# Optimization experiments

Hardware: AMD Instinct MI355X
Metric: run time of the kernel (lower is better)

The kernel has to match this reference:

```python
import jax, jax.numpy as jnp
import numpy as np

NEG_SLOPE = 0.2  # PyG GATConv default negative_slope
BN_EPS = 1e-5


def _segment_softmax(logits, seg, num_segments):
    # numerically stable softmax over edges grouped by destination node
    m = jax.ops.segment_max(logits, seg, num_segments=num_segments)
    e = jnp.exp(logits - m[seg])
    s = jax.ops.segment_sum(e, seg, num_segments=num_segments)
    return e / s[seg]


def _gat_conv(x, src, dst, W, a_src, a_dst, bias, heads, d_head, concat):
    N = x.shape[0]
    h = (x @ W).reshape(N, heads, d_head)                      # [N, H, D]
    alpha_src = jnp.einsum('nhd,hd->nh', h, a_src)             # [N, H]
    alpha_dst = jnp.einsum('nhd,hd->nh', h, a_dst)             # [N, H]
    logits = jax.nn.leaky_relu(alpha_src[src] + alpha_dst[dst], NEG_SLOPE)  # [E, H]
    alpha = _segment_softmax(logits, dst, N)                   # [E, H]
    msg = h[src] * alpha[:, :, None]                           # [E, H, D]
    out = jax.ops.segment_sum(msg, dst, num_segments=N)        # [N, H, D]
    out = out.reshape(N, heads * d_head) if concat else out.mean(axis=1)
    return out + bias


def setup_inputs() -> dict:
    key = jax.random.key(0)
    ks = jax.random.split(key, 12)
    N, E = 50000, 800000
    in_dim, hidden, out_dim, heads = 256, 128, 2, 4
    d1 = hidden // heads  # 32
    s = 0.05
    return {
        'x': jax.random.normal(ks[0], (N, in_dim), dtype=jnp.float32),
        'edge_index': jax.random.randint(ks[1], (2, E), 0, N, dtype=jnp.int64),
        'W1': jax.random.normal(ks[2], (in_dim, heads * d1), dtype=jnp.float32) * s,
        'att_src1': jax.random.normal(ks[3], (heads, d1), dtype=jnp.float32) * s,
        'att_dst1': jax.random.normal(ks[4], (heads, d1), dtype=jnp.float32) * s,
        'b1': jnp.zeros((heads * d1,), dtype=jnp.float32),
        'bn_gamma': jnp.ones((hidden,), dtype=jnp.float32),
        'bn_beta': jnp.zeros((hidden,), dtype=jnp.float32),
        'bn_mean': jnp.zeros((hidden,), dtype=jnp.float32),
        'bn_var': jnp.ones((hidden,), dtype=jnp.float32),
        'W2': jax.random.normal(ks[5], (hidden, out_dim), dtype=jnp.float32) * s,
        'att_src2': jax.random.normal(ks[6], (1, out_dim), dtype=jnp.float32) * s,
        'att_dst2': jax.random.normal(ks[7], (1, out_dim), dtype=jnp.float32) * s,
        'b2': jnp.zeros((out_dim,), dtype=jnp.float32),
    }


def reference(x, edge_index, W1, att_src1, att_dst1, b1,
              bn_gamma, bn_beta, bn_mean, bn_var,
              W2, att_src2, att_dst2, b2):
    N = x.shape[0]
    # PyG GATConv adds self-loops by default
    loop = jnp.arange(N, dtype=edge_index.dtype)
    src = jnp.concatenate([edge_index[0], loop])
    dst = jnp.concatenate([edge_index[1], loop])

    heads, d1 = att_src1.shape
    h = _gat_conv(x, src, dst, W1, att_src1, att_dst1, b1, heads, d1, concat=True)
    # BatchNorm1d in eval mode (running stats), then ReLU (dropout is a no-op in eval)
    h = (h - bn_mean) * jax.lax.rsqrt(bn_var + BN_EPS) * bn_gamma + bn_beta
    h = jax.nn.relu(h)
    out = _gat_conv(h, src, dst, W2, att_src2, att_dst2, b2, 1, att_src2.shape[1], concat=False)
    return out
```

## Files before the change

### kernel.cpp

```cpp
#include <hip/hip_runtime.h>
#include <hip/hip_bf16.h>

#define LRELU(x) ((x) > 0.f ? (x) : 0.2f * (x))
#define CAP 96
#define BINBITS 7
#define BINCAP 2600

typedef short bf16x8 __attribute__((ext_vector_type(8)));
typedef float f32x4 __attribute__((ext_vector_type(4)));

__device__ __forceinline__ float b2f(unsigned short u) {
  union { unsigned int i; float f; } v;
  v.i = ((unsigned int)u) << 16;
  return v.f;
}
__device__ __forceinline__ unsigned short f2b(float f) {
  unsigned int u = __float_as_uint(f);
  unsigned int r = (u + 0x7fffu + ((u >> 16) & 1u)) >> 16;
  return (unsigned short)r;
}

__device__ __forceinline__ void acc2(float w, unsigned int p, float& a0,
                                     float& a1) {
  union { unsigned int u; float f; } lo, hi;
  lo.u = p << 16;
  hi.u = p & 0xffff0000u;
  a0 = fmaf(w, lo.f, a0);
  a1 = fmaf(w, hi.f, a1);
}

__global__ __launch_bounds__(256) void prep_w1t_kernel(
    const float* __restrict__ W, unsigned short* __restrict__ w1t) {
  int idx = blockIdx.x * 256 + threadIdx.x;
  int n = idx >> 8, k = idx & 255;
  w1t[idx] = f2b(W[k * 128 + n]);
}

__global__ __launch_bounds__(256) void gemm1_mfma_kernel(
    const float* __restrict__ x, const unsigned short* __restrict__ w1t,
    const float* __restrict__ atts, const float* __restrict__ attd,
    unsigned short* __restrict__ h1bf, float* __restrict__ asrc,
    float* __restrict__ adst, int N) {
  __shared__ unsigned short bsh[128 * 264];

  const int tid = threadIdx.x;
#pragma unroll
  for (int i = 0; i < 16; i++) {
    int idx = (i * 256 + tid) * 8;
    int row = idx >> 8;
    int k = idx & 255;
    *(uint4*)(bsh + row * 264 + k) = *(const uint4*)(w1t + row * 256 + k);
  }
  __syncthreads();

  const int m0 = blockIdx.x * 64 + (tid >> 6) * 16;
  if (m0 >= N) return;
  const int lane = tid & 63;
  const int row = lane & 15;
  const int quad = lane >> 4;

  f32x4 acc[8];
#pragma unroll
  for (int t = 0; t < 8; t++) acc[t] = (f32x4){0.f, 0.f, 0.f, 0.f};

  const float* ap = x + (size_t)(m0 + row) * 256 + quad * 8;
#pragma unroll
  for (int k0 = 0; k0 < 256; k0 += 32) {
    float4 av0 = *(const float4*)(ap + k0);
    float4 av1 = *(const float4*)(ap + k0 + 4);
    float af[8] = {av0.x, av0.y, av0.z, av0.w, av1.x, av1.y, av1.z, av1.w};
    bf16x8 ahi, alo;
#pragma unroll
    for (int j = 0; j < 8; j++) {
      unsigned short h = f2b(af[j]);
      ahi[j] = (short)h;
      alo[j] = (short)f2b(af[j] - b2f(h));
    }
#pragma unroll
    for (int t = 0; t < 8; t++) {
      bf16x8 b = *(const bf16x8*)(bsh + (t * 16 + row) * 264 + k0 + quad * 8);
      acc[t] = __builtin_amdgcn_mfma_f32_16x16x32_bf16(ahi, b, acc[t], 0, 0, 0);
      acc[t] = __builtin_amdgcn_mfma_f32_16x16x32_bf16(alo, b, acc[t], 0, 0, 0);
    }
  }
  unsigned short* op = h1bf + (size_t)(m0 + quad * 4) * 128 + row;
#pragma unroll
  for (int t = 0; t < 8; t++)
#pragma unroll
    for (int r = 0; r < 4; r++)
      op[(size_t)r * 128 + t * 16] = f2b(acc[t][r]);

  float asv[8], adv[8];
#pragma unroll
  for (int t = 0; t < 8; t++) {
    asv[t] = atts[t * 16 + row];
    adv[t] = attd[t * 16 + row];
  }
  float ps[4][4], pd[4][4];
#pragma unroll
  for (int h = 0; h < 4; h++)
#pragma unroll
    for (int r = 0; r < 4; r++) {
      ps[h][r] = acc[2 * h][r] * asv[2 * h] + acc[2 * h + 1][r] * asv[2 * h + 1];
      pd[h][r] = acc[2 * h][r] * adv[2 * h] + acc[2 * h + 1][r] * adv[2 * h + 1];
    }
#pragma unroll
  for (int o = 1; o < 16; o <<= 1) {
#pragma unroll
    for (int h = 0; h < 4; h++)
#pragma unroll
      for (int r = 0; r < 4; r++) {
        ps[h][r] += __shfl_xor(ps[h][r], o);
        pd[h][r] += __shfl_xor(pd[h][r], o);
      }
  }
  if (row == 0) {
#pragma unroll
    for (int r = 0; r < 4; r++) {
      int m = m0 + quad * 4 + r;
#pragma unroll
      for (int h = 0; h < 4; h++) {
        asrc[m * 4 + h] = ps[h][r];
        adst[m * 4 + h] = pd[h][r];
      }
    }
  }
}

__global__ __launch_bounds__(256) void bin_edges_kernel(
    const int* __restrict__ ei, int E, int* __restrict__ gcnt,
    unsigned int* __restrict__ binned, int nbins) {
  __shared__ int hist[512];
  __shared__ int base[512];
  const int tid = threadIdx.x;
  for (int i = tid; i < 512; i += 256) hist[i] = 0;
  __syncthreads();
  const int chunk = (E + gridDim.x - 1) / gridDim.x;
  const int e0 = blockIdx.x * chunk;
  const int e1 = min(e0 + chunk, E);
  for (int e = e0 + tid; e < e1; e += 256)
    atomicAdd(&hist[ei[(size_t)E + e] >> BINBITS], 1);
  __syncthreads();
  for (int i = tid; i < nbins; i += 256)
    if (hist[i] > 0) base[i] = atomicAdd(&gcnt[i], hist[i]);
  __syncthreads();
  for (int i = tid; i < 512; i += 256) hist[i] = 0;
  __syncthreads();
  for (int e = e0 + tid; e < e1; e += 256) {
    int s = ei[e];
    int t = ei[(size_t)E + e];
    int b = t >> BINBITS;
    int pos = base[b] + atomicAdd(&hist[b], 1);
    if (pos < BINCAP)
      binned[(size_t)b * BINCAP + pos] = ((unsigned int)t << 16) | (unsigned int)s;
  }
}

__global__ __launch_bounds__(256) void bin_to_buckets_kernel(
    const int* __restrict__ gcnt, const unsigned int* __restrict__ binned,
    int* __restrict__ cnt, unsigned short* __restrict__ buckets, int N) {
  __shared__ unsigned short lbkt[128 * CAP];
  __shared__ int lcnt[128];
  const int b = blockIdx.x;
  const int tid = threadIdx.x;
  if (tid < 128) lcnt[tid] = 0;
  __syncthreads();
  const int ne = min(gcnt[b], BINCAP);
  const unsigned int* bp = binned + (size_t)b * BINCAP;
  for (int i = tid; i < ne; i += 256) {
    unsigned int p = bp[i];
    int ln = (p >> 16) & 127;
    int pos = atomicAdd(&lcnt[ln], 1);
    if (pos < CAP) lbkt[ln * CAP + pos] = (unsigned short)(p & 0xffff);
  }
  __syncthreads();
  const int n0 = b << BINBITS;
  const int nn = min(128, N - n0);
  if (nn <= 0) return;
  if (tid < nn) cnt[n0 + tid] = lcnt[tid];
  const int total8 = (nn * CAP) >> 3;
  uint4* d4 = (uint4*)(buckets + (size_t)n0 * CAP);
  const uint4* s4 = (const uint4*)lbkt;
  for (int i = tid; i < total8; i += 256) d4[i] = s4[i];
}

__global__ __launch_bounds__(256) void agg1_kernel(
    const int* __restrict__ cnt, const unsigned short* __restrict__ buckets,
    const unsigned short* __restrict__ h1bf, const float* __restrict__ asrc,
    const float* __restrict__ adst, const float* __restrict__ b1,
    const float* __restrict__ gamma, const float* __restrict__ beta,
    const float* __restrict__ mean, const float* __restrict__ var,
    const float* __restrict__ W2, const float* __restrict__ as2,
    const float* __restrict__ ad2, float4* __restrict__ pk, int N) {
  __shared__ float wsh[4][4][100];
  const int wv = __builtin_amdgcn_readfirstlane(threadIdx.x >> 6);
  const int t = blockIdx.x * 4 + wv;
  if (t >= N) return;
  const int l = threadIdx.x & 63;
  const int h = l >> 4;
  const int js = l & 15;
  const float ad = adst[t * 4 + h];

  const unsigned short* bkt = buckets + (size_t)t * CAP;
  const int deg = min(__builtin_amdgcn_readfirstlane(cnt[t]), CAP);

  float* wrow = &wsh[wv][h][0];
  float denp = 0.f;
  const int nb = (deg + 15) >> 4;
  for (int b = 0; b < nb; b++) {
    const int idx = (b << 4) + js;
    const int s = (int)bkt[idx];
    const float av = asrc[s * 4 + h];
    float w = __expf(LRELU(av + ad));
    w = (idx < deg) ? w : 0.f;
    wrow[idx] = w;
    denp += w;
  }
#pragma unroll
  for (int o = 1; o < 16; o <<= 1) denp += __shfl_xor(denp, o);
  const float wself = __expf(LRELU(asrc[t * 4 + h] + ad));
  const float den = denp + wself;

  float acc0 = 0.f, acc1 = 0.f;
  int j = 0;
  for (; j + 8 <= deg; j += 8) {
    const uint4 e4 = *(const uint4*)(bkt + j);
    const unsigned int ea = __builtin_amdgcn_readfirstlane(e4.x);
    const unsigned int eb = __builtin_amdgcn_readfirstlane(e4.y);
    const unsigned int ec = __builtin_amdgcn_readfirstlane(e4.z);
    const unsigned int ed = __builtin_amdgcn_readfirstlane(e4.w);
    const int s0 = ea & 0xffff, s1 = ea >> 16;
    const int s2 = eb & 0xffff, s3 = eb >> 16;
    const int s4 = ec & 0xffff, s5 = ec >> 16;
    const int s6 = ed & 0xffff, s7 = ed >> 16;
    const unsigned int p0 = *(const unsigned int*)(h1bf + (size_t)s0 * 128 + 2 * l);
    const unsigned int p1 = *(const unsigned int*)(h1bf + (size_t)s1 * 128 + 2 * l);
    const unsigned int p2 = *(const unsigned int*)(h1bf + (size_t)s2 * 128 + 2 * l);
    const unsigned int p3 = *(const unsigned int*)(h1bf + (size_t)s3 * 128 + 2 * l);
    const unsigned int p4 = *(const unsigned int*)(h1bf + (size_t)s4 * 128 + 2 * l);
    const unsigned int p5 = *(const unsigned int*)(h1bf + (size_t)s5 * 128 + 2 * l);
    const unsigned int p6 = *(const unsigned int*)(h1bf + (size_t)s6 * 128 + 2 * l);
    const unsigned int p7 = *(const unsigned int*)(h1bf + (size_t)s7 * 128 + 2 * l);
    const f32x4 wa = *(const f32x4*)(wrow + j);
    const f32x4 wb = *(const f32x4*)(wrow + j + 4);
    acc2(wa[0], p0, acc0, acc1);
    acc2(wa[1], p1, acc0, acc1);
    acc2(wa[2], p2, acc0, acc1);
    acc2(wa[3], p3, acc0, acc1);
    acc2(wb[0], p4, acc0, acc1);
    acc2(wb[1], p5, acc0, acc1);
    acc2(wb[2], p6, acc0, acc1);
    acc2(wb[3], p7, acc0, acc1);
  }
  for (; j + 4 <= deg; j += 4) {
    const uint2 e2v = *(const uint2*)(bkt + j);
    const unsigned int ea = __builtin_amdgcn_readfirstlane(e2v.x);
    const unsigned int eb = __builtin_amdgcn_readfirstlane(e2v.y);
    const int s0 = ea & 0xffff, s1 = ea >> 16;
    const int s2 = eb & 0xffff, s3 = eb >> 16;
    const unsigned int p0 = *(const unsigned int*)(h1bf + (size_t)s0 * 128 + 2 * l);
    const unsigned int p1 = *(const unsigned int*)(h1bf + (size_t)s1 * 128 + 2 * l);
    const unsigned int p2 = *(const unsigned int*)(h1bf + (size_t)s2 * 128 + 2 * l);
    const unsigned int p3 = *(const unsigned int*)(h1bf + (size_t)s3 * 128 + 2 * l);
    const f32x4 wa = *(const f32x4*)(wrow + j);
    acc2(wa[0], p0, acc0, acc1);
    acc2(wa[1], p1, acc0, acc1);
    acc2(wa[2], p2, acc0, acc1);
    acc2(wa[3], p3, acc0, acc1);
  }
  for (; j < deg; j++) {
    const int s0 = __builtin_amdgcn_readfirstlane((int)bkt[j]);
    const unsigned int p0 = *(const unsigned int*)(h1bf + (size_t)s0 * 128 + 2 * l);
    acc2(wrow[j], p0, acc0, acc1);
  }
  {
    const unsigned int p0 = *(const unsigned int*)(h1bf + (size_t)t * 128 + 2 * l);
    acc2(wself, p0, acc0, acc1);
  }

  const int c0 = 2 * l;
  float inv = 1.f / den;
  float v0 = acc0 * inv + b1[c0];
  float v1 = acc1 * inv + b1[c0 + 1];
  v0 = (v0 - mean[c0]) * rsqrtf(var[c0] + 1e-5f) * gamma[c0] + beta[c0];
  v1 = (v1 - mean[c0 + 1]) * rsqrtf(var[c0 + 1] + 1e-5f) * gamma[c0 + 1] +
       beta[c0 + 1];
  v0 = v0 > 0.f ? v0 : 0.f;
  v1 = v1 > 0.f ? v1 : 0.f;

  float g0 = v0 * W2[c0 * 2 + 0] + v1 * W2[(c0 + 1) * 2 + 0];
  float g1 = v0 * W2[c0 * 2 + 1] + v1 * W2[(c0 + 1) * 2 + 1];
#pragma unroll
  for (int o = 32; o > 0; o >>= 1) {
    g0 += __shfl_down(g0, o);
    g1 += __shfl_down(g1, o);
  }
  if (l == 0) {
    float4 p;
    p.x = g0;
    p.y = g1;
    p.z = g0 * as2[0] + g1 * as2[1];
    p.w = g0 * ad2[0] + g1 * ad2[1];
    pk[t] = p;
  }
}

__global__ __launch_bounds__(256) void agg2_kernel(
    const int* __restrict__ cnt, const unsigned short* __restrict__ buckets,
    const float4* __restrict__ pk, const float* __restrict__ b2,
    float* __restrict__ out, int N) {
  const int t = blockIdx.x * 16 + (threadIdx.x >> 4);
  if (t >= N) return;
  const int lg = threadIdx.x & 15;
  float4 pt = pk[t];
  const float ad = pt.w;
  float a0 = 0.f, a1 = 0.f, den = 0.f;
  const unsigned short* bkt = buckets + (size_t)t * CAP;
  const int deg = min(cnt[t], CAP);
  for (int j = lg; j < deg; j += 16) {
    float4 p = pk[bkt[j]];
    float w = __expf(LRELU(p.z + ad));
    a0 += w * p.x;
    a1 += w * p.y;
    den += w;
  }
#pragma unroll
  for (int o = 8; o > 0; o >>= 1) {
    a0 += __shfl_xor(a0, o);
    a1 += __shfl_xor(a1, o);
    den += __shfl_xor(den, o);
  }
  if (lg == 0) {
    float w = __expf(LRELU(pt.z + ad));
    a0 += w * pt.x;
    a1 += w * pt.y;
    den += w;
    float2 o2;
    o2.x = a0 / den + b2[0];
    o2.y = a1 / den + b2[1];
    *(float2*)(out + (size_t)t * 2) = o2;
  }
}

extern "C" void kernel_launch(void* const* d_in, const int* in_sizes, int n_in,
                              void* d_out, int out_size, void* d_ws,
                              size_t ws_size, hipStream_t stream) {
  const float* x      = (const float*)d_in[0];
  const int*   ei     = (const int*)d_in[1];
  const float* W1     = (const float*)d_in[2];
  const float* atts1  = (const float*)d_in[3];
  const float* attd1  = (const float*)d_in[4];
  const float* b1     = (const float*)d_in[5];
  const float* gamma  = (const float*)d_in[6];
  const float* beta   = (const float*)d_in[7];
  const float* mean   = (const float*)d_in[8];
  const float* var    = (const float*)d_in[9];
  const float* W2     = (const float*)d_in[10];
  const float* atts2  = (const float*)d_in[11];
  const float* attd2  = (const float*)d_in[12];
  const float* b2     = (const float*)d_in[13];
  float* out = (float*)d_out;

  const int N = in_sizes[0] / 256;
  const int E = in_sizes[1] / 2;
  const int nbins = (N + (1 << BINBITS) - 1) >> BINBITS;

  char* ws = (char*)d_ws;
  size_t off = 0;
  unsigned short* h1bf = (unsigned short*)(ws + off); off += (size_t)N * 128 * 2;
  float* asrc1 = (float*)(ws + off); off += (size_t)N * 4 * 4;
  float* adst1 = (float*)(ws + off); off += (size_t)N * 4 * 4;
  float4* pk   = (float4*)(ws + off); off += (size_t)N * 16;
  int*   cnt   = (int*)  (ws + off); off += (size_t)N * 4;
  int*   gcnt  = (int*)  (ws + off); off += 512 * 4;
  unsigned short* w1t = (unsigned short*)(ws + off); off += 128 * 256 * 2;
  unsigned short* buckets = (unsigned short*)(ws + off);
  off += (size_t)N * CAP * 2;
  unsigned int* binned = (unsigned int*)(ws + off);
  off += (size_t)nbins * BINCAP * 4;

  hipMemsetAsync(gcnt, 0, 512 * 4, stream);
  bin_edges_kernel<<<512, 256, 0, stream>>>(ei, E, gcnt, binned, nbins);
  bin_to_buckets_kernel<<<nbins, 256, 0, stream>>>(gcnt, binned, cnt, buckets,
                                                   N);

  prep_w1t_kernel<<<128, 256, 0, stream>>>(W1, w1t);
  gemm1_mfma_kernel<<<(N + 63) / 64, 256, 0, stream>>>(
      x, w1t, atts1, attd1, h1bf, asrc1, adst1, N);
  agg1_kernel<<<(N + 3) / 4, 256, 0, stream>>>(cnt, buckets, h1bf, asrc1,
                                               adst1, b1, gamma, beta, mean,
                                               var, W2, atts2, attd2, pk, N);

  agg2_kernel<<<(N + 15) / 16, 256, 0, stream>>>(cnt, buckets, pk, b2, out, N);
}
```

Measured before the change: 201.1 us.

## Prefetch neighbor gathers in registers and broadcast softmax weights via shuffles

Rewrites the layer-1 aggregation so that the first 32 neighbor feature gathers are issued before the softmax weight computation, hiding gather latency. Attention weights stay in registers and are broadcast with lane shuffles instead of going through shared memory, and the main loop processes fixed blocks of 16 edges padded with zero weights. BatchNorm, bias and W2 parameters are loaded as vectors up front and folded into a single scale and offset. The trade-off is higher register use from the 32-entry prefetch array and extra gathers of padding entries (clamped to valid rows) when the degree is not a multiple of 16.

```diff
diff --git a/kernel.cpp b/kernel.cpp
--- a/kernel.cpp
+++ b/kernel.cpp
@@ -192,116 +192,138 @@
     const float* __restrict__ mean, const float* __restrict__ var,
     const float* __restrict__ W2, const float* __restrict__ as2,
     const float* __restrict__ ad2, float4* __restrict__ pk, int N) {
-  __shared__ float wsh[4][4][100];
   const int wv = __builtin_amdgcn_readfirstlane(threadIdx.x >> 6);
   const int t = blockIdx.x * 4 + wv;
   if (t >= N) return;
   const int l = threadIdx.x & 63;
   const int h = l >> 4;
   const int js = l & 15;
+  const int c0 = 2 * l;
+  const int wsrc = l & 48;
+
+  const float2 b1v = *(const float2*)(b1 + c0);
+  const float2 mv = *(const float2*)(mean + c0);
+  const float2 vv = *(const float2*)(var + c0);
+  const float2 gv = *(const float2*)(gamma + c0);
+  const float2 bb = *(const float2*)(beta + c0);
+  const float4 w2v = *(const float4*)(W2 + c0 * 2);
+  const float as20 = as2[0], as21 = as2[1];
+  const float ad20 = ad2[0], ad21 = ad2[1];
+
   const float ad = adst[t * 4 + h];
+  const float aself = asrc[t * 4 + h];
 
   const unsigned short* bkt = buckets + (size_t)t * CAP;
   const int deg = min(__builtin_amdgcn_readfirstlane(cnt[t]), CAP);
-
-  float* wrow = &wsh[wv][h][0];
+  const int nb = (deg + 15) >> 4;
+  const int nmax = N - 1;
+
+  unsigned int p[32];
+  int sa[32];
+#define EXTR2(word, i)                                              \
+  {                                                                 \
+    unsigned int u_ = __builtin_amdgcn_readfirstlane(word);         \
+    sa[i] = min((int)(u_ & 0xffffu), nmax);                         \
+    sa[i + 1] = min((int)(u_ >> 16), nmax);                         \
+  }
+#define LOAD8(ea, eb, base)                                         \
+  {                                                                 \
+    EXTR2((ea).x, base + 0)                                         \
+    EXTR2((ea).y, base + 2)                                         \
+    EXTR2((ea).z, base + 4)                                         \
+    EXTR2((ea).w, base + 6)                                         \
+    _Pragma("unroll") for (int i_ = 0; i_ < 8; i_++) p[base + i_] = \
+        *(const unsigned int*)(h1bf + (size_t)sa[base + i_] * 128 + c0); \
+    (void)(eb);                                                     \
+  }
+
+  if (deg > 0) {
+    const uint4 ea0 = *(const uint4*)(bkt);
+    const uint4 eb0 = *(const uint4*)(bkt + 8);
+    LOAD8(ea0, ea0, 0)
+    LOAD8(eb0, eb0, 8)
+    if (deg > 16) {
+      const uint4 ea1 = *(const uint4*)(bkt + 16);
+      const uint4 eb1 = *(const uint4*)(bkt + 24);
+      LOAD8(ea1, ea1, 16)
+      LOAD8(eb1, eb1, 24)
+    }
+  }
+
+  float wb[6];
   float denp = 0.f;
-  const int nb = (deg + 15) >> 4;
-  for (int b = 0; b < nb; b++) {
-    const int idx = (b << 4) + js;
-    const int s = (int)bkt[idx];
-    const float av = asrc[s * 4 + h];
-    float w = __expf(LRELU(av + ad));
-    w = (idx < deg) ? w : 0.f;
-    wrow[idx] = w;
+#pragma unroll
+  for (int b = 0; b < 6; b++) {
+    float w = 0.f;
+    if (b < nb) {
+      const int idx = (b << 4) + js;
+      const int s = (int)bkt[idx];
+      const float av = asrc[s * 4 + h];
+      w = __expf(LRELU(av + ad));
+      w = (idx < deg) ? w : 0.f;
+    }
+    wb[b] = w;
     denp += w;
   }
 #pragma unroll
   for (int o = 1; o < 16; o <<= 1) denp += __shfl_xor(denp, o);
-  const float wself = __expf(LRELU(asrc[t * 4 + h] + ad));
+  const float wself = __expf(LRELU(aself + ad));
   const float den = denp + wself;
 
   float acc0 = 0.f, acc1 = 0.f;
-  int j = 0;
-  for (; j + 8 <= deg; j += 8) {
-    const uint4 e4 = *(const uint4*)(bkt + j);
-    const unsigned int ea = __builtin_amdgcn_readfirstlane(e4.x);
-    const unsigned int eb = __builtin_amdgcn_readfirstlane(e4.y);
-    const unsigned int ec = __builtin_amdgcn_readfirstlane(e4.z);
-    const unsigned int ed = __builtin_amdgcn_readfirstlane(e4.w);
-    const int s0 = ea & 0xffff, s1 = ea >> 16;
-    const int s2 = eb & 0xffff, s3 = eb >> 16;
-    const int s4 = ec & 0xffff, s5 = ec >> 16;
-    const int s6 = ed & 0xffff, s7 = ed >> 16;
-    const unsigned int p0 = *(const unsigned int*)(h1bf + (size_t)s0 * 128 + 2 * l);
-    const unsigned int p1 = *(const unsigned int*)(h1bf + (size_t)s1 * 128 + 2 * l);
-    const unsigned int p2 = *(const unsigned int*)(h1bf + (size_t)s2 * 128 + 2 * l);
-    const unsigned int p3 = *(const unsigned int*)(h1bf + (size_t)s3 * 128 + 2 * l);
-    const unsigned int p4 = *(const unsigned int*)(h1bf + (size_t)s4 * 128 + 2 * l);
-    const unsigned int p5 = *(const unsigned int*)(h1bf + (size_t)s5 * 128 + 2 * l);
-    const unsigned int p6 = *(const unsigned int*)(h1bf + (size_t)s6 * 128 + 2 * l);
-    const unsigned int p7 = *(const unsigned int*)(h1bf + (size_t)s7 * 128 + 2 * l);
-    const f32x4 wa = *(const f32x4*)(wrow + j);
-    const f32x4 wb = *(const f32x4*)(wrow + j + 4);
-    acc2(wa[0], p0, acc0, acc1);
-    acc2(wa[1], p1, acc0, acc1);
-    acc2(wa[2], p2, acc0, acc1);
-    acc2(wa[3], p3, acc0, acc1);
-    acc2(wb[0], p4, acc0, acc1);
-    acc2(wb[1], p5, acc0, acc1);
-    acc2(wb[2], p6, acc0, acc1);
-    acc2(wb[3], p7, acc0, acc1);
-  }
-  for (; j + 4 <= deg; j += 4) {
-    const uint2 e2v = *(const uint2*)(bkt + j);
-    const unsigned int ea = __builtin_amdgcn_readfirstlane(e2v.x);
-    const unsigned int eb = __builtin_amdgcn_readfirstlane(e2v.y);
-    const int s0 = ea & 0xffff, s1 = ea >> 16;
-    const int s2 = eb & 0xffff, s3 = eb >> 16;
-    const unsigned int p0 = *(const unsigned int*)(h1bf + (size_t)s0 * 128 + 2 * l);
-    const unsigned int p1 = *(const unsigned int*)(h1bf + (size_t)s1 * 128 + 2 * l);
-    const unsigned int p2 = *(const unsigned int*)(h1bf + (size_t)s2 * 128 + 2 * l);
-    const unsigned int p3 = *(const unsigned int*)(h1bf + (size_t)s3 * 128 + 2 * l);
-    const f32x4 wa = *(const f32x4*)(wrow + j);
-    acc2(wa[0], p0, acc0, acc1);
-    acc2(wa[1], p1, acc0, acc1);
-    acc2(wa[2], p2, acc0, acc1);
-    acc2(wa[3], p3, acc0, acc1);
-  }
-  for (; j < deg; j++) {
-    const int s0 = __builtin_amdgcn_readfirstlane((int)bkt[j]);
-    const unsigned int p0 = *(const unsigned int*)(h1bf + (size_t)s0 * 128 + 2 * l);
-    acc2(wrow[j], p0, acc0, acc1);
+  if (deg > 0) {
+#pragma unroll
+    for (int j = 0; j < 16; j++)
+      acc2(__shfl(wb[0], wsrc + j), p[j], acc0, acc1);
+    if (deg > 16) {
+#pragma unroll
+      for (int j = 0; j < 16; j++)
+        acc2(__shfl(wb[1], wsrc + j), p[16 + j], acc0, acc1);
+    }
+  }
+#pragma unroll
+  for (int b = 2; b < 6; b++) {
+    if (deg > (b << 4)) {
+      const uint4 ea = *(const uint4*)(bkt + (b << 4));
+      const uint4 eb = *(const uint4*)(bkt + (b << 4) + 8);
+      LOAD8(ea, ea, 0)
+      LOAD8(eb, eb, 8)
+#pragma unroll
+      for (int j = 0; j < 16; j++)
+        acc2(__shfl(wb[b], wsrc + j), p[j], acc0, acc1);
+    }
   }
   {
-    const unsigned int p0 = *(const unsigned int*)(h1bf + (size_t)t * 128 + 2 * l);
+    const unsigned int p0 = *(const unsigned int*)(h1bf + (size_t)t * 128 + c0);
     acc2(wself, p0, acc0, acc1);
   }
-
-  const int c0 = 2 * l;
-  float inv = 1.f / den;
-  float v0 = acc0 * inv + b1[c0];
-  float v1 = acc1 * inv + b1[c0 + 1];
-  v0 = (v0 - mean[c0]) * rsqrtf(var[c0] + 1e-5f) * gamma[c0] + beta[c0];
-  v1 = (v1 - mean[c0 + 1]) * rsqrtf(var[c0 + 1] + 1e-5f) * gamma[c0 + 1] +
-       beta[c0 + 1];
+#undef EXTR2
+#undef LOAD8
+
+  const float sc0 = rsqrtf(vv.x + 1e-5f) * gv.x;
+  const float sc1 = rsqrtf(vv.y + 1e-5f) * gv.y;
+  const float of0 = (b1v.x - mv.x) * sc0 + bb.x;
+  const float of1 = (b1v.y - mv.y) * sc1 + bb.y;
+  const float inv = 1.f / den;
+  float v0 = fmaf(acc0 * inv, sc0, of0);
+  float v1 = fmaf(acc1 * inv, sc1, of1);
   v0 = v0 > 0.f ? v0 : 0.f;
   v1 = v1 > 0.f ? v1 : 0.f;
 
-  float g0 = v0 * W2[c0 * 2 + 0] + v1 * W2[(c0 + 1) * 2 + 0];
-  float g1 = v0 * W2[c0 * 2 + 1] + v1 * W2[(c0 + 1) * 2 + 1];
+  float g0 = v0 * w2v.x + v1 * w2v.z;
+  float g1 = v0 * w2v.y + v1 * w2v.w;
 #pragma unroll
   for (int o = 32; o > 0; o >>= 1) {
     g0 += __shfl_down(g0, o);
     g1 += __shfl_down(g1, o);
   }
   if (l == 0) {
-    float4 p;
-    p.x = g0;
-    p.y = g1;
-    p.z = g0 * as2[0] + g1 * as2[1];
-    p.w = g0 * ad2[0] + g1 * ad2[1];
-    pk[t] = p;
+    float4 p4;
+    p4.x = g0;
+    p4.y = g1;
+    p4.z = g0 * as20 + g1 * as21;
+    p4.w = g0 * ad20 + g1 * ad21;
+    pk[t] = p4;
   }
 }
 
```

After: 209.5 us. 1.04x slower.
